# Performance work log

Hardware: AMD Instinct MI355X
Metric: run time of the kernel (lower is better)

Reference implementation:

```python
import jax, jax.numpy as jnp
import numpy as np
from jax import lax

# Static config (mirrors Caps2dMatwo init_kwargs)
K_SIZE = 5
T1 = 8              # num_capsule (output capsule types)
POS = (4, 4)
APP = (4, 4)
ROUTINGS = 3
COORD_ADD = True
ZP = POS[0] * POS[1]   # 16
ZA = APP[0] * APP[1]   # 16
Z = ZP + ZA            # 32 == input channels z_0


def _psquash(p, axis):
    return p / jnp.max(jnp.abs(p), axis=axis, keepdims=True)


def _matwo_squash(p, axis):
    n2 = jnp.sum(p * p, axis=axis, keepdims=True)
    n = jnp.sqrt(n2 + 1e-9)
    return n2 / (1.0 + n2) * p / n


def _coord_const(H, W):
    # coordinate_addition: adds normalized (x, y) into last row of the pos matrix
    yy, xx = np.meshgrid(np.arange(H), np.arange(W), indexing='ij')
    c = np.zeros((H * W, 1, POS[1], POS[1]), np.float32)
    c[:, 0, -1, 0] = xx.reshape(-1) / W
    c[:, 0, -1, 1] = yy.reshape(-1) / H
    return jnp.asarray(c)


def setup_inputs() -> dict:
    key = jax.random.key(0)
    k1, k2, k3, k4, k5 = jax.random.split(key, 5)
    N, T0, H, W = 4, 4, 96, 96
    return {
        'input_tensor': jax.random.normal(k1, (N, T0, Z, H, W), jnp.float32),
        'W_conv': jax.random.normal(k2, (T0, K_SIZE, K_SIZE, 1, T1), jnp.float32) * 0.05,
        'W_pos': jax.random.normal(k3, (T0, POS[1] * POS[1], T1), jnp.float32) * 0.05,
        'W_app': jax.random.normal(k4, (T0, APP[1] * APP[1], T1), jnp.float32) * 0.05,
        'b_app': jax.random.normal(k5, (T0, T1), jnp.float32) * 0.05,
    }


def reference(input_tensor, W_conv, W_pos, W_app, b_app):
    N, t0, z0, H, W = input_tensor.shape
    coord = _coord_const(H, W)
    u_hat_list = []
    for i in range(t0):
        # per input capsule type: spatial conv applied channel-wise
        u_t = input_tensor[:, i].reshape(N * z0, H, W, 1)
        u_spat = lax.conv_general_dilated(
            u_t, W_conv[i], (1, 1), 'SAME',
            dimension_numbers=('NHWC', 'HWIO', 'NHWC'))        # [N*z0, H, W, T1]
        u_spat = (u_spat.reshape(N, z0, H, W, T1)
                  .transpose(0, 2, 3, 4, 1)                    # [N,H,W,T1,z0]
                  .reshape(N, H, W, T1 * z0))
        u_pos = u_spat[..., :T1 * ZP].reshape(N, H, W, T1, POS[0], POS[1])
        u_app = u_spat[..., T1 * ZP:].reshape(N, H, W, T1, APP[0], APP[1])
        m_pos = W_pos[i].reshape(T1, POS[1], POS[1])
        m_app = W_app[i].reshape(T1, APP[1], APP[1])
        u_app = u_app + b_app[i].reshape(1, 1, 1, T1, 1, 1)
        # l2 normalize pos matrix along axis -2 (tf.l2_normalize semantics)
        m_pos = m_pos / jnp.sqrt(jnp.maximum(
            jnp.sum(m_pos * m_pos, axis=-2, keepdims=True), 1e-12))
        if COORD_ADD:
            m_pos = (m_pos + coord).reshape(1, H, W, T1, POS[1], POS[1])
        # matmult2d == batched matmul
        u_hat_pos = jnp.matmul(u_pos, m_pos).reshape(N, H, W, T1, ZP)
        u_hat_app = jnp.matmul(u_app, m_app).reshape(N, H, W, T1, ZA)
        u_hat_t = jnp.concatenate([u_hat_pos, u_hat_app], axis=-1)
        u_hat_list.append(u_hat_t.transpose(0, 4, 1, 2, 3))    # [N,Z,H,W,T1]
    u_hat = jnp.stack(u_hat_list, axis=-2)                     # [N,Z,H,W,t0,T1]

    # dual routing (sigmoid agreement), vectorized across output capsules
    u_pos_all = u_hat[:, :ZP]
    u_app_all = u_hat[:, ZP:]
    b = jnp.zeros((N, H, W, t0, T1), input_tensor.dtype)
    for _ in range(ROUTINGS - 1):
        r = jax.nn.sigmoid(b)                                  # [N,H,W,t0,T1]
        p = jnp.einsum('nzhwot,nhwot->tnzhw', u_hat, r)        # [T1,N,Z,H,W]
        v_pos = _psquash(p[:, :, :ZP], 2)
        v_app = _matwo_squash(p[:, :, ZP:], 2)
        rout = (jnp.einsum('nzhwot,tnzhw->nhwot', u_pos_all, v_pos)
                * jnp.einsum('nzhwot,tnzhw->nhwot', u_app_all, v_app))
        b = b + rout
    c = jax.nn.sigmoid(b)

    p = jnp.einsum('nzhwot,nhwot->tnzhw', u_hat, c)
    v_pos = _psquash(p[:, :, :ZP], 2)
    v_app = _matwo_squash(p[:, :, ZP:], 2)
    out = jnp.concatenate([v_pos, v_app], axis=2)              # [T1,N,Z,H,W]
    return out.transpose(1, 0, 2, 3, 4)                        # [N,T1,Z,H,W]
```

## Files before the change

### kernel.cpp

```cpp
#include <hip/hip_runtime.h>
#include <hip/hip_fp16.h>
#include <math.h>

#define IMG_H 96
#define IMG_W 96
#define HW (IMG_H * IMG_W)
#define TW 16
#define TH 2
#define TR (TH + 4)
#define TC 20
#define TS2 36

__device__ __forceinline__ float quad_sum(float v) {
    v += __int_as_float(__builtin_amdgcn_update_dpp(
            0, __float_as_int(v), 0xB1, 0xF, 0xF, true));
    v += __int_as_float(__builtin_amdgcn_update_dpp(
            0, __float_as_int(v), 0x4E, 0xF, 0xF, true));
    return v;
}
__device__ __forceinline__ float quad_max(float v) {
    v = fmaxf(v, __int_as_float(__builtin_amdgcn_update_dpp(
            0, __float_as_int(v), 0xB1, 0xF, 0xF, true)));
    v = fmaxf(v, __int_as_float(__builtin_amdgcn_update_dpp(
            0, __float_as_int(v), 0x4E, 0xF, 0xF, true)));
    return v;
}

__device__ __forceinline__ void route_store(const float (*uh)[8], int q, int nt,
                                            int pix, float* __restrict__ out)
{
    float bb[4] = {0.0f, 0.0f, 0.0f, 0.0f};
    #pragma unroll
    for (int it = 0; it < 2; ++it) {
        float r0 = 1.0f / (1.0f + __expf(-bb[0]));
        float r1 = 1.0f / (1.0f + __expf(-bb[1]));
        float r2 = 1.0f / (1.0f + __expf(-bb[2]));
        float r3 = 1.0f / (1.0f + __expf(-bb[3]));
        float pz[4], pa[4];
        #pragma unroll
        for (int j = 0; j < 4; ++j)
            pz[j] = fmaf(uh[0][j], r0, fmaf(uh[1][j], r1,
                    fmaf(uh[2][j], r2, uh[3][j] * r3)));
        float mx = quad_max(fmaxf(fmaxf(fabsf(pz[0]), fabsf(pz[1])),
                                  fmaxf(fabsf(pz[2]), fabsf(pz[3]))));
        float dp[4];
        #pragma unroll
        for (int o = 0; o < 4; ++o)
            dp[o] = quad_sum(fmaf(uh[o][0], pz[0], fmaf(uh[o][1], pz[1],
                             fmaf(uh[o][2], pz[2], uh[o][3] * pz[3]))));
        #pragma unroll
        for (int j = 0; j < 4; ++j)
            pa[j] = fmaf(uh[0][4 + j], r0, fmaf(uh[1][4 + j], r1,
                    fmaf(uh[2][4 + j], r2, uh[3][4 + j] * r3)));
        float n2 = quad_sum(fmaf(pa[0], pa[0], fmaf(pa[1], pa[1],
                            fmaf(pa[2], pa[2], pa[3] * pa[3]))));
        float invm = 1.0f / mx;
        float sc   = n2 / ((1.0f + n2) * sqrtf(n2 + 1e-9f));
        #pragma unroll
        for (int o = 0; o < 4; ++o) {
            float da = quad_sum(fmaf(uh[o][4], pa[0], fmaf(uh[o][5], pa[1],
                               fmaf(uh[o][6], pa[2], uh[o][7] * pa[3]))));
            bb[o] += (invm * dp[o]) * (sc * da);
        }
    }
    float r0 = 1.0f / (1.0f + __expf(-bb[0]));
    float r1 = 1.0f / (1.0f + __expf(-bb[1]));
    float r2 = 1.0f / (1.0f + __expf(-bb[2]));
    float r3 = 1.0f / (1.0f + __expf(-bb[3]));
    float pz[4], pa[4];
    #pragma unroll
    for (int j = 0; j < 4; ++j)
        pz[j] = fmaf(uh[0][j], r0, fmaf(uh[1][j], r1,
                fmaf(uh[2][j], r2, uh[3][j] * r3)));
    float mx = quad_max(fmaxf(fmaxf(fabsf(pz[0]), fabsf(pz[1])),
                              fmaxf(fabsf(pz[2]), fabsf(pz[3]))));
    #pragma unroll
    for (int j = 0; j < 4; ++j)
        pa[j] = fmaf(uh[0][4 + j], r0, fmaf(uh[1][4 + j], r1,
                fmaf(uh[2][4 + j], r2, uh[3][4 + j] * r3)));
    float n2 = quad_sum(fmaf(pa[0], pa[0], fmaf(pa[1], pa[1],
                        fmaf(pa[2], pa[2], pa[3] * pa[3]))));
    float invm = 1.0f / mx;
    float sc   = n2 / ((1.0f + n2) * sqrtf(n2 + 1e-9f));
    float* op = out + ((size_t)nt * 32 + (q << 2)) * HW + pix;
    op[0 * HW] = pz[0] * invm;
    op[1 * HW] = pz[1] * invm;
    op[2 * HW] = pz[2] * invm;
    op[3 * HW] = pz[3] * invm;
    op[16 * HW] = pa[0] * sc;
    op[17 * HW] = pa[1] * sc;
    op[18 * HW] = pa[2] * sc;
    op[19 * HW] = pa[3] * sc;
}

__global__ void __launch_bounds__(512)
caps_one_kernel(const float* __restrict__ x,
                const float* __restrict__ Wc,
                const float* __restrict__ Wp,
                const float* __restrict__ Wa,
                const float* __restrict__ Ba,
                float* __restrict__ out)
{
    __shared__ __align__(16) __half2 tile2[TR * TC * TS2];
    __shared__ __align__(16) __half2 wpk[400];
    __shared__ __align__(16) float   msh[512];
    __shared__ __align__(16) float   ash[512];

    const int tid    = threadIdx.x;
    const int q      = tid & 3;
    const int px     = (tid >> 2) & 15;
    const int wv     = tid >> 6;
    const int rr     = wv >> 2;
    const int wb     = blockIdx.x * TW;
    const int h0     = blockIdx.y * TH;
    const int n      = blockIdx.z >> 1;
    const int parity = blockIdx.z & 1;
    const int t      = parity + 2 * (wv & 3);
    const int w      = wb + px;
    const int h      = h0 + rr;

    for (int i = tid; i < 400; i += 512) {
        int fp  = i / 100;
        int rem = i - fp * 100;
        int tap = rem >> 2;
        int g   = i & 3;
        int oe  = (g & 1) << 1;
        int f   = fp + ((g >> 1) << 2);
        wpk[i] = __floats2half2_rn(Wc[oe * 200 + tap * 8 + f],
                                   Wc[(oe + 1) * 200 + tap * 8 + f]);
    }
    if (tid < 128) {
        int c  = tid & 3;
        int tt = (tid >> 2) & 7;
        int oo = tid >> 5;
        const float* src = Wp + oo * 128 + tt * 16 + c;
        float v0 = src[0], v1 = src[4], v2 = src[8], v3 = src[12];
        float s = v0 * v0 + v1 * v1 + v2 * v2 + v3 * v3;
        float inv = 1.0f / sqrtf(fmaxf(s, 1e-12f));
        float* dst = msh + (oo * 8 + tt) * 16 + c;
        dst[0] = v0 * inv; dst[4] = v1 * inv; dst[8] = v2 * inv; dst[12] = v3 * inv;
    } else if (tid < 256) {
        int i = tid - 128;
        ((float4*)ash)[i] = ((const float4*)Wa)[i];
    }
    {
        const int col = tid & 15;
        const int g   = tid >> 4;
        #pragma unroll
        for (int k = 0; k < 2; ++k) {
            int r = g + (k << 5);
            if (r < 48) {
                int dy    = r >> 3;
                int cpg   = r & 7;
                int hh    = h0 + dy - 2;
                int zq    = cpg >> 1;
                int cbase = (cpg & 1) << 1;
                int chan  = n * 128 + parity * 16 + zq * 4 + cbase;
                float v[8];
                #pragma unroll
                for (int j = 0; j < 8; ++j) v[j] = 0.0f;
                if ((unsigned)hh < IMG_H) {
                    const float* src = x + (size_t)chan * HW + hh * IMG_W + wb + col;
                    #pragma unroll
                    for (int j = 0; j < 8; ++j)
                        v[j] = src[(size_t)((j & 3) * 32 + (j >> 2)) * HW];
                }
                __half2 h4[4];
                #pragma unroll
                for (int j = 0; j < 4; ++j)
                    h4[j] = __floats2half2_rn(v[2 * j], v[2 * j + 1]);
                *(uint4*)&tile2[(dy * TC + 2 + col) * TS2 + (cpg << 2)] =
                    *(const uint4*)h4;
            }
        }
        const int m  = tid & 3;
        const int xx = (m < 2) ? m : (m + TW);
        const int ww = wb - 2 + xx;
        const int rh = tid >> 2;
        #pragma unroll
        for (int k = 0; k < 2; ++k) {
            int r = rh + (k << 7);
            if (r < 192) {
                int dy = r >> 5;
                int cp = r & 31;
                int hh = h0 + dy - 2;
                int o0 = (cp & 1) << 1;
                int c  = (cp >> 1) & 3;
                int zq = cp >> 3;
                int chan = n * 128 + o0 * 32 + parity * 16 + zq * 4 + c;
                float v0 = 0.0f, v1 = 0.0f;
                if ((unsigned)hh < IMG_H && (unsigned)ww < IMG_W) {
                    const float* src = x + (size_t)chan * HW + hh * IMG_W + ww;
                    v0 = src[0];
                    v1 = src[(size_t)32 * HW];
                }
                tile2[(dy * TC + xx) * TS2 + cp] = __floats2half2_rn(v0, v1);
            }
        }
    }
    __syncthreads();

    __half2 rp2[8], ra2[8];
    const __half2 z2 = __float2half2_rn(0.0f);
    #pragma unroll
    for (int i = 0; i < 8; ++i) { rp2[i] = z2; ra2[i] = z2; }

    const uint4* wb4 = (const uint4*)&wpk[(t >> 1) * 100];
    #pragma unroll 1
    for (int dy = 0; dy < 5; ++dy) {
        #pragma unroll
        for (int dx = 0; dx < 5; ++dx) {
            const __half2* t2 =
                &tile2[((rr + dy) * TC + px + dx) * TS2 + (q << 3)];
            union { uint4 u; __half2 hh[4]; } A, B, Wt;
            A.u  = *(const uint4*)t2;
            B.u  = *(const uint4*)(t2 + 4);
            Wt.u = wb4[dy * 5 + dx];
            rp2[0] = __hfma2(A.hh[0], Wt.hh[0], rp2[0]);
            rp2[1] = __hfma2(A.hh[1], Wt.hh[1], rp2[1]);
            rp2[2] = __hfma2(A.hh[2], Wt.hh[0], rp2[2]);
            rp2[3] = __hfma2(A.hh[3], Wt.hh[1], rp2[3]);
            rp2[4] = __hfma2(B.hh[0], Wt.hh[0], rp2[4]);
            rp2[5] = __hfma2(B.hh[1], Wt.hh[1], rp2[5]);
            rp2[6] = __hfma2(B.hh[2], Wt.hh[0], rp2[6]);
            rp2[7] = __hfma2(B.hh[3], Wt.hh[1], rp2[7]);
            ra2[0] = __hfma2(A.hh[0], Wt.hh[2], ra2[0]);
            ra2[1] = __hfma2(A.hh[1], Wt.hh[3], ra2[1]);
            ra2[2] = __hfma2(A.hh[2], Wt.hh[2], ra2[2]);
            ra2[3] = __hfma2(A.hh[3], Wt.hh[3], ra2[3]);
            ra2[4] = __hfma2(B.hh[0], Wt.hh[2], ra2[4]);
            ra2[5] = __hfma2(B.hh[1], Wt.hh[3], ra2[5]);
            ra2[6] = __hfma2(B.hh[2], Wt.hh[2], ra2[6]);
            ra2[7] = __hfma2(B.hh[3], Wt.hh[3], ra2[7]);
        }
    }

    float uh[4][8];
    {
        const float cx = (float)w * (1.0f / 96.0f);
        const float cy = (float)h * (1.0f / 96.0f);
        #pragma unroll
        for (int o = 0; o < 4; ++o) {
            const float* mb = &msh[(o * 8 + t) * 16];
            float4 m0 = *(const float4*)(mb + 0);
            float4 m1 = *(const float4*)(mb + 4);
            float4 m2 = *(const float4*)(mb + 8);
            float4 m3 = *(const float4*)(mb + 12);
            m3.x += cx;
            m3.y += cy;
            const int pr = o >> 1;
            float r0, r1, r2, r3;
            if (o & 1) {
                r0 = __high2float(rp2[0 + pr]); r1 = __high2float(rp2[2 + pr]);
                r2 = __high2float(rp2[4 + pr]); r3 = __high2float(rp2[6 + pr]);
            } else {
                r0 = __low2float(rp2[0 + pr]);  r1 = __low2float(rp2[2 + pr]);
                r2 = __low2float(rp2[4 + pr]);  r3 = __low2float(rp2[6 + pr]);
            }
            uh[o][0] = r0 * m0.x + r1 * m1.x + r2 * m2.x + r3 * m3.x;
            uh[o][1] = r0 * m0.y + r1 * m1.y + r2 * m2.y + r3 * m3.y;
            uh[o][2] = r0 * m0.z + r1 * m1.z + r2 * m2.z + r3 * m3.z;
            uh[o][3] = r0 * m0.w + r1 * m1.w + r2 * m2.w + r3 * m3.w;
        }
        #pragma unroll
        for (int o = 0; o < 4; ++o) {
            const float* ab = &ash[(o * 8 + t) * 16];
            float4 a0 = *(const float4*)(ab + 0);
            float4 a1 = *(const float4*)(ab + 4);
            float4 a2 = *(const float4*)(ab + 8);
            float4 a3 = *(const float4*)(ab + 12);
            const float bias = Ba[o * 8 + t];
            const int pr = o >> 1;
            float r0, r1, r2, r3;
            if (o & 1) {
                r0 = __high2float(ra2[0 + pr]); r1 = __high2float(ra2[2 + pr]);
                r2 = __high2float(ra2[4 + pr]); r3 = __high2float(ra2[6 + pr]);
            } else {
                r0 = __low2float(ra2[0 + pr]);  r1 = __low2float(ra2[2 + pr]);
                r2 = __low2float(ra2[4 + pr]);  r3 = __low2float(ra2[6 + pr]);
            }
            r0 += bias; r1 += bias; r2 += bias; r3 += bias;
            uh[o][4] = r0 * a0.x + r1 * a1.x + r2 * a2.x + r3 * a3.x;
            uh[o][5] = r0 * a0.y + r1 * a1.y + r2 * a2.y + r3 * a3.y;
            uh[o][6] = r0 * a0.z + r1 * a1.z + r2 * a2.z + r3 * a3.z;
            uh[o][7] = r0 * a0.w + r1 * a1.w + r2 * a2.w + r3 * a3.w;
        }
    }

    route_store(uh, q, n * 8 + t, h * IMG_W + w, out);
}

extern "C" void kernel_launch(void* const* d_in, const int* in_sizes, int n_in,
                              void* d_out, int out_size, void* d_ws, size_t ws_size,
                              hipStream_t stream) {
    const float* x  = (const float*)d_in[0];
    const float* Wc = (const float*)d_in[1];
    const float* Wp = (const float*)d_in[2];
    const float* Wa = (const float*)d_in[3];
    const float* Ba = (const float*)d_in[4];
    float* outp = (float*)d_out;

    caps_one_kernel<<<dim3(IMG_W / TW, IMG_H / TH, 8), 512, 0, stream>>>(
        x, Wc, Wp, Wa, Ba, outp);
}
```

Before: 126.8 us.

## Move weight packing into a separate pre-kernel and read packed weights from global

Result: no change. 125.3 us (-1.2%).

```diff
diff --git a/kernel.cpp b/kernel.cpp
--- a/kernel.cpp
+++ b/kernel.cpp
@@ -10,6 +10,9 @@
 #define TR (TH + 4)
 #define TC 20
 #define TS2 36
+
+#define WS_MSH 400
+#define WS_ASH 912
 
 __device__ __forceinline__ float quad_sum(float v) {
     v += __int_as_float(__builtin_amdgcn_update_dpp(
@@ -93,41 +96,21 @@
     op[19 * HW] = pa[3] * sc;
 }
 
-__global__ void __launch_bounds__(512)
-caps_one_kernel(const float* __restrict__ x,
-                const float* __restrict__ Wc,
-                const float* __restrict__ Wp,
-                const float* __restrict__ Wa,
-                const float* __restrict__ Ba,
-                float* __restrict__ out)
+__global__ void __launch_bounds__(256)
+caps_pack_kernel(const float* __restrict__ Wc, const float* __restrict__ Wp,
+                 const float* __restrict__ Wa, float* __restrict__ ws)
 {
-    __shared__ __align__(16) __half2 tile2[TR * TC * TS2];
-    __shared__ __align__(16) __half2 wpk[400];
-    __shared__ __align__(16) float   msh[512];
-    __shared__ __align__(16) float   ash[512];
-
-    const int tid    = threadIdx.x;
-    const int q      = tid & 3;
-    const int px     = (tid >> 2) & 15;
-    const int wv     = tid >> 6;
-    const int rr     = wv >> 2;
-    const int wb     = blockIdx.x * TW;
-    const int h0     = blockIdx.y * TH;
-    const int n      = blockIdx.z >> 1;
-    const int parity = blockIdx.z & 1;
-    const int t      = parity + 2 * (wv & 3);
-    const int w      = wb + px;
-    const int h      = h0 + rr;
-
-    for (int i = tid; i < 400; i += 512) {
+    const int tid = threadIdx.x;
+    for (int i = tid; i < 400; i += 256) {
         int fp  = i / 100;
         int rem = i - fp * 100;
         int tap = rem >> 2;
         int g   = i & 3;
         int oe  = (g & 1) << 1;
         int f   = fp + ((g >> 1) << 2);
-        wpk[i] = __floats2half2_rn(Wc[oe * 200 + tap * 8 + f],
-                                   Wc[(oe + 1) * 200 + tap * 8 + f]);
+        __half2 hv = __floats2half2_rn(Wc[oe * 200 + tap * 8 + f],
+                                       Wc[(oe + 1) * 200 + tap * 8 + f]);
+        ((__half2*)ws)[i] = hv;
     }
     if (tid < 128) {
         int c  = tid & 3;
@@ -137,12 +120,35 @@
         float v0 = src[0], v1 = src[4], v2 = src[8], v3 = src[12];
         float s = v0 * v0 + v1 * v1 + v2 * v2 + v3 * v3;
         float inv = 1.0f / sqrtf(fmaxf(s, 1e-12f));
-        float* dst = msh + (oo * 8 + tt) * 16 + c;
+        float* dst = ws + WS_MSH + (oo * 8 + tt) * 16 + c;
         dst[0] = v0 * inv; dst[4] = v1 * inv; dst[8] = v2 * inv; dst[12] = v3 * inv;
-    } else if (tid < 256) {
+    } else {
         int i = tid - 128;
-        ((float4*)ash)[i] = ((const float4*)Wa)[i];
-    }
+        ((float4*)(ws + WS_ASH))[i] = ((const float4*)Wa)[i];
+    }
+}
+
+__global__ void __launch_bounds__(512)
+caps_one_kernel(const float* __restrict__ x,
+                const float* __restrict__ ws,
+                const float* __restrict__ Ba,
+                float* __restrict__ out)
+{
+    __shared__ __align__(16) __half2 tile2[TR * TC * TS2];
+
+    const int tid    = threadIdx.x;
+    const int q      = tid & 3;
+    const int px     = (tid >> 2) & 15;
+    const int wv     = tid >> 6;
+    const int wb     = blockIdx.x * TW;
+    const int h0     = blockIdx.y * TH;
+    const int n      = blockIdx.z >> 1;
+    const int parity = blockIdx.z & 1;
+    const int t      = __builtin_amdgcn_readfirstlane(parity + 2 * (wv & 3));
+    const int rr     = __builtin_amdgcn_readfirstlane(wv >> 2);
+    const int w      = wb + px;
+    const int h      = h0 + rr;
+
     {
         const int col = tid & 15;
         const int g   = tid >> 4;
@@ -205,7 +211,7 @@
     #pragma unroll
     for (int i = 0; i < 8; ++i) { rp2[i] = z2; ra2[i] = z2; }
 
-    const uint4* wb4 = (const uint4*)&wpk[(t >> 1) * 100];
+    const uint4* wq = (const uint4*)ws + (t >> 1) * 25;
     #pragma unroll 1
     for (int dy = 0; dy < 5; ++dy) {
         #pragma unroll
@@ -215,7 +221,7 @@
             union { uint4 u; __half2 hh[4]; } A, B, Wt;
             A.u  = *(const uint4*)t2;
             B.u  = *(const uint4*)(t2 + 4);
-            Wt.u = wb4[dy * 5 + dx];
+            Wt.u = wq[dy * 5 + dx];
             rp2[0] = __hfma2(A.hh[0], Wt.hh[0], rp2[0]);
             rp2[1] = __hfma2(A.hh[1], Wt.hh[1], rp2[1]);
             rp2[2] = __hfma2(A.hh[2], Wt.hh[0], rp2[2]);
@@ -241,7 +247,7 @@
         const float cy = (float)h * (1.0f / 96.0f);
         #pragma unroll
         for (int o = 0; o < 4; ++o) {
-            const float* mb = &msh[(o * 8 + t) * 16];
+            const float* mb = ws + WS_MSH + (o * 8 + t) * 16;
             float4 m0 = *(const float4*)(mb + 0);
             float4 m1 = *(const float4*)(mb + 4);
             float4 m2 = *(const float4*)(mb + 8);
@@ -264,7 +270,7 @@
         }
         #pragma unroll
         for (int o = 0; o < 4; ++o) {
-            const float* ab = &ash[(o * 8 + t) * 16];
+            const float* ab = ws + WS_ASH + (o * 8 + t) * 16;
             float4 a0 = *(const float4*)(ab + 0);
             float4 a1 = *(const float4*)(ab + 4);
             float4 a2 = *(const float4*)(ab + 8);
@@ -299,7 +305,9 @@
     const float* Wa = (const float*)d_in[3];
     const float* Ba = (const float*)d_in[4];
     float* outp = (float*)d_out;
-
+    float* ws   = (float*)d_ws;
+
+    caps_pack_kernel<<<dim3(1), 256, 0, stream>>>(Wc, Wp, Wa, ws);
     caps_one_kernel<<<dim3(IMG_W / TW, IMG_H / TH, 8), 512, 0, stream>>>(
-        x, Wc, Wp, Wa, Ba, outp);
-}
+        x, ws, Ba, outp);
+}
```
